# Optimization experiments

Hardware: AMD Instinct MI355X
Metric: run time of the kernel (lower is better)

Reference implementation:

```python
import jax, jax.numpy as jnp
import numpy as np


def setup_inputs() -> dict:
    key = jax.random.key(0)
    kK, kQ = jax.random.split(key)
    B, S, D = 8, 2048, 512
    K = jax.random.normal(kK, (B, S, D), dtype=jnp.float32)
    Q = jax.random.normal(kQ, (B, S, D), dtype=jnp.float32)
    return {"K": K, "Q": Q}


def reference(K, Q):
    # K: [B, S_k, D], Q: [B, S_q, D]
    S_q = Q.shape[1]
    S_k = K.shape[1]
    # Causal mask: -inf strictly above the diagonal (k=1), as in np.triu(..., k=1)
    mask = jnp.where(jnp.triu(jnp.ones((S_q, S_k), dtype=bool), k=1), -jnp.inf, 0.0).astype(jnp.float32)
    # NOTE: original scales by sqrt(window_size_keys) (seq len), and adds mask BEFORE scaling.
    logits = (jnp.einsum('bqd,bkd->bqk', Q, K) + mask) / jnp.sqrt(jnp.float32(S_k))
    return jax.nn.softmax(logits, axis=-1)
```

## Files before the change

### kernel.cpp

```cpp
#include <hip/hip_runtime.h>
#include <hip/hip_bf16.h>
#include <math.h>

#define B_SZ 8
#define SEQ 2048
#define DIM 512

typedef __attribute__((ext_vector_type(8))) short bf16x8;
typedef __attribute__((ext_vector_type(8))) unsigned short u16x8;
typedef __attribute__((ext_vector_type(4))) float f32x4;

#define GLOBAL_AS __attribute__((address_space(1)))
#define LDS_AS __attribute__((address_space(3)))

__device__ __forceinline__ unsigned short f2bf(float f) {
    unsigned int u = __builtin_bit_cast(unsigned int, f);
    u += 0x7fffu + ((u >> 16) & 1u);
    return (unsigned short)(u >> 16);
}

__device__ __forceinline__ void load_lds16(const void* g, void* l) {
    __builtin_amdgcn_global_load_lds((const GLOBAL_AS unsigned int*)g,
                                     (LDS_AS unsigned int*)l, 16, 0, 0);
}

__global__ __launch_bounds__(256)
void convert_kernel(const float* __restrict__ Q, const float* __restrict__ K,
                    unsigned short* __restrict__ Qb, unsigned short* __restrict__ Kb,
                    float* __restrict__ sums) {
    const int half = (int)(((size_t)B_SZ * SEQ * DIM) / 8 / 256);
    const int bid = blockIdx.x;
    const int gi = bid * 256 + threadIdx.x;
    if (gi < B_SZ * SEQ) sums[gi] = 0.f;

    const float* src;
    unsigned short* dst;
    int i;
    if (bid < half) { src = Q; dst = Qb; i = gi; }
    else            { src = K; dst = Kb; i = gi - half * 256; }

    const float4* s = (const float4*)src;
    float4 a = s[2 * i];
    float4 b = s[2 * i + 1];
    u16x8 o;
    o[0] = f2bf(a.x); o[1] = f2bf(a.y); o[2] = f2bf(a.z); o[3] = f2bf(a.w);
    o[4] = f2bf(b.x); o[5] = f2bf(b.y); o[6] = f2bf(b.z); o[7] = f2bf(b.w);
    ((u16x8*)dst)[i] = o;
}

#define BM 128
#define BK 32
__global__ __launch_bounds__(256)
void logits_exp_mfma(const unsigned short* __restrict__ Qb, const unsigned short* __restrict__ Kb,
                     float* __restrict__ out, float* __restrict__ sums) {
    const int b = blockIdx.x, tk = blockIdx.y, tq = blockIdx.z;
    float* outb = out + (size_t)b * SEQ * SEQ;
    const int t = threadIdx.x;

    if (tk > tq) {
        const int r0 = t >> 5;
        const int c4 = t & 31;
        const float4 z = {0.f, 0.f, 0.f, 0.f};
        float* base = outb + (size_t)(tq * BM) * SEQ + tk * BM;
#pragma unroll
        for (int it = 0; it < 16; ++it)
            *(float4*)(base + (size_t)(it * 8 + r0) * SEQ + c4 * 4) = z;
        return;
    }

    __shared__ __align__(16) unsigned short a_lds[BM * BK];
    __shared__ __align__(16) unsigned short b_lds[BM * BK];

    const int wave = t >> 6;
    const int lane = t & 63;
    const int l16 = lane & 15;
    const int quad = lane >> 4;
    const int wm = wave >> 1;
    const int wn = wave & 1;

    const unsigned short* Qrow = Qb + ((size_t)b * SEQ + (size_t)tq * BM) * DIM;
    const unsigned short* Krow = Kb + ((size_t)b * SEQ + (size_t)tk * BM) * DIM;

    const int sr = lane >> 2;
    const int kg = lane & 3;
    const int gsw = kg ^ ((sr >> 1) & 3);

    f32x4 acc[4][4];
#pragma unroll
    for (int i = 0; i < 4; i++)
#pragma unroll
        for (int j = 0; j < 4; j++) acc[i][j] = (f32x4){0.f, 0.f, 0.f, 0.f};

    for (int k0 = 0; k0 < DIM; k0 += BK) {
#pragma unroll
        for (int j = wave; j < 8; j += 4) {
            int row = j * 16 + sr;
            load_lds16(Qrow + (size_t)row * DIM + k0 + gsw * 8, &a_lds[(j * 16) * BK]);
            load_lds16(Krow + (size_t)row * DIM + k0 + gsw * 8, &b_lds[(j * 16) * BK]);
        }
        __syncthreads();

        bf16x8 af[4], bfr[4];
#pragma unroll
        for (int mi = 0; mi < 4; mi++) {
            const int row = wm * 64 + mi * 16 + l16;
            const int slot = quad ^ ((row >> 1) & 3);
            af[mi] = *(const bf16x8*)&a_lds[row * BK + slot * 8];
        }
#pragma unroll
        for (int ni = 0; ni < 4; ni++) {
            const int row = wn * 64 + ni * 16 + l16;
            const int slot = quad ^ ((row >> 1) & 3);
            bfr[ni] = *(const bf16x8*)&b_lds[row * BK + slot * 8];
        }
#pragma unroll
        for (int mi = 0; mi < 4; mi++)
#pragma unroll
            for (int ni = 0; ni < 4; ni++)
                acc[mi][ni] = __builtin_amdgcn_mfma_f32_16x16x32_bf16(af[mi], bfr[ni], acc[mi][ni], 0, 0, 0);
        __syncthreads();
    }

    const float scale = 0.02209708691207961f;
    const bool diag = (tk == tq);
    float* sums_b = sums + (size_t)b * SEQ;

#pragma unroll
    for (int mi = 0; mi < 4; mi++) {
#pragma unroll
        for (int r = 0; r < 4; r++) {
            const int row_l = wm * 64 + mi * 16 + quad * 4 + r;
            const int row = tq * BM + row_l;
            float rsum = 0.f;
#pragma unroll
            for (int ni = 0; ni < 4; ni++) {
                const int col = tk * BM + wn * 64 + ni * 16 + l16;
                float e;
                if (diag && col > row) e = 0.f;
                else e = __expf(acc[mi][ni][r] * scale);
                outb[(size_t)row * SEQ + col] = e;
                rsum += e;
            }
            rsum += __shfl_xor(rsum, 1);
            rsum += __shfl_xor(rsum, 2);
            rsum += __shfl_xor(rsum, 4);
            rsum += __shfl_xor(rsum, 8);
            if (l16 == 0) atomicAdd(&sums_b[row], rsum);
        }
    }
}

__global__ __launch_bounds__(256)
void scale_kernel(float* __restrict__ out, const float* __restrict__ sums) {
    const int q = blockIdx.x & (SEQ - 1);
    const int b = blockIdx.x >> 11;
    float* row = out + ((size_t)b * SEQ + q) * SEQ;
    const float inv = 1.0f / sums[blockIdx.x];
    const int n = q + 1;
    const int t = threadIdx.x;
#pragma unroll
    for (int j = 0; j < 2; ++j) {
        int k0 = (t + j * 256) * 4;
        if (k0 < n) {
            float4 x = *(const float4*)(row + k0);
            x.x *= inv; x.y *= inv; x.z *= inv; x.w *= inv;
            *(float4*)(row + k0) = x;
        }
    }
}

#define TS 64
#define DC 128
#define LSTRIDE (DC + 8)
__global__ __launch_bounds__(256)
void logits_fallback(const float* __restrict__ Q, const float* __restrict__ K,
                     float* __restrict__ out) {
    const int tk = blockIdx.x, tq = blockIdx.y, b = blockIdx.z;
    if (tk > tq) return;
    __shared__ __align__(16) unsigned short qs[TS * LSTRIDE];
    __shared__ __align__(16) unsigned short ks[TS * LSTRIDE];
    const int t = threadIdx.x;
    const int wave = t >> 6, lane = t & 63, l16 = lane & 15, quad = lane >> 4;
    const float* Qb = Q + ((size_t)b * SEQ + (size_t)tq * TS) * DIM;
    const float* Kb = K + ((size_t)b * SEQ + (size_t)tk * TS) * DIM;
    f32x4 acc[4];
#pragma unroll
    for (int i = 0; i < 4; i++) acc[i] = (f32x4){0.f, 0.f, 0.f, 0.f};
    for (int c = 0; c < DIM; c += DC) {
        __syncthreads();
#pragma unroll
        for (int i = 0; i < 8; i++) {
            int idx = t + i * 256;
            int row = idx >> 5, c4 = idx & 31;
            float4 qv = *(const float4*)(Qb + row * DIM + c + c4 * 4);
            float4 kv = *(const float4*)(Kb + row * DIM + c + c4 * 4);
            ushort4 qh = { f2bf(qv.x), f2bf(qv.y), f2bf(qv.z), f2bf(qv.w) };
            ushort4 kh = { f2bf(kv.x), f2bf(kv.y), f2bf(kv.z), f2bf(kv.w) };
            *(ushort4*)&qs[row * LSTRIDE + c4 * 4] = qh;
            *(ushort4*)&ks[row * LSTRIDE + c4 * 4] = kh;
        }
        __syncthreads();
#pragma unroll
        for (int d = 0; d < DC; d += 32) {
            bf16x8 afrag = *(const bf16x8*)&qs[(wave * 16 + l16) * LSTRIDE + d + quad * 8];
#pragma unroll
            for (int nt = 0; nt < 4; nt++) {
                bf16x8 bfrag = *(const bf16x8*)&ks[(nt * 16 + l16) * LSTRIDE + d + quad * 8];
                acc[nt] = __builtin_amdgcn_mfma_f32_16x16x32_bf16(afrag, bfrag, acc[nt], 0, 0, 0);
            }
        }
    }
    const float scale = 0.02209708691207961f;
    float* outb = out + (size_t)b * SEQ * SEQ;
#pragma unroll
    for (int nt = 0; nt < 4; nt++) {
        int col = tk * TS + nt * 16 + l16;
#pragma unroll
        for (int r = 0; r < 4; r++) {
            int row = tq * TS + wave * 16 + quad * 4 + r;
            outb[(size_t)row * SEQ + col] = acc[nt][r] * scale;
        }
    }
}

__global__ __launch_bounds__(256)
void softmax_kernel(float* __restrict__ out) {
    const int q = blockIdx.x & (SEQ - 1);
    const int b = blockIdx.x >> 11;
    float* row = out + ((size_t)b * SEQ + q) * SEQ;
    const int t = threadIdx.x;
    const int lane = t & 63;
    const int wave = t >> 6;
    const int n = q + 1;

    __shared__ float red[8];

    float4 v[2];
    float m = -INFINITY;
#pragma unroll
    for (int j = 0; j < 2; j++) {
        int k0 = (t + j * 256) * 4;
        if (k0 < n) {
            float4 x = *(const float4*)(row + k0);
            x.y = (k0 + 1 < n) ? x.y : -INFINITY;
            x.z = (k0 + 2 < n) ? x.z : -INFINITY;
            x.w = (k0 + 3 < n) ? x.w : -INFINITY;
            v[j] = x;
            m = fmaxf(m, fmaxf(fmaxf(x.x, x.y), fmaxf(x.z, x.w)));
        } else {
            v[j] = (float4){-INFINITY, -INFINITY, -INFINITY, -INFINITY};
        }
    }
#pragma unroll
    for (int off = 1; off < 64; off <<= 1) m = fmaxf(m, __shfl_xor(m, off));
    if (lane == 0) red[wave] = m;
    __syncthreads();
    m = fmaxf(fmaxf(red[0], red[1]), fmaxf(red[2], red[3]));

    float s = 0.f;
#pragma unroll
    for (int j = 0; j < 2; j++) {
        float4 e;
        e.x = __expf(v[j].x - m);
        e.y = __expf(v[j].y - m);
        e.z = __expf(v[j].z - m);
        e.w = __expf(v[j].w - m);
        v[j] = e;
        s += e.x + e.y + e.z + e.w;
    }
#pragma unroll
    for (int off = 1; off < 64; off <<= 1) s += __shfl_xor(s, off);
    if (lane == 0) red[4 + wave] = s;
    __syncthreads();
    s = red[4] + red[5] + red[6] + red[7];
    const float inv = 1.0f / s;

#pragma unroll
    for (int j = 0; j < 2; j++) {
        int k0 = (t + j * 256) * 4;
        float4 e = v[j];
        e.x *= inv; e.y *= inv; e.z *= inv; e.w *= inv;
        *(float4*)(row + k0) = e;
    }
}

extern "C" void kernel_launch(void* const* d_in, const int* in_sizes, int n_in,
                              void* d_out, int out_size, void* d_ws, size_t ws_size,
                              hipStream_t stream) {
    const float* Kp = (const float*)d_in[0];
    const float* Qp = (const float*)d_in[1];
    float* out = (float*)d_out;

    const size_t nElem = (size_t)B_SZ * SEQ * DIM;
    const size_t bfBytes = nElem * sizeof(unsigned short);
    const size_t sumsBytes = (size_t)B_SZ * SEQ * sizeof(float);

    if (ws_size >= 2 * bfBytes + sumsBytes) {
        unsigned short* Qbf = (unsigned short*)d_ws;
        unsigned short* Kbf = Qbf + nElem;
        float* sums = (float*)((char*)d_ws + 2 * bfBytes);
        const int half = (int)(nElem / 8 / 256);
        convert_kernel<<<dim3(2 * half), dim3(256), 0, stream>>>(Qp, Kp, Qbf, Kbf, sums);
        logits_exp_mfma<<<dim3(B_SZ, SEQ / BM, SEQ / BM), dim3(256), 0, stream>>>(Qbf, Kbf, out, sums);
        scale_kernel<<<dim3(B_SZ * SEQ), dim3(256), 0, stream>>>(out, sums);
    } else {
        logits_fallback<<<dim3(SEQ / TS, SEQ / TS, B_SZ), dim3(256), 0, stream>>>(Qp, Kp, out);
        softmax_kernel<<<dim3(B_SZ * SEQ), dim3(256), 0, stream>>>(out);
    }
}
```

Baseline: 227.4 us.

## Double-buffer LDS tiles to overlap global loads with MFMA compute

Turns the single LDS staging buffer for the Q and K tiles into a double buffer. The next K-slice is prefetched with global_load_lds while MFMAs run on the current slice, and a partial vmcnt wait (4 loads outstanding) replaces the full __syncthreads wait. This aims to hide global-memory latency in the GEMM main loop, at the cost of twice the LDS use, which may reduce occupancy. It also relies on hand-written waitcnt and barrier ordering being correct.

```diff
diff --git a/kernel.cpp b/kernel.cpp
--- a/kernel.cpp
+++ b/kernel.cpp
@@ -68,8 +68,8 @@
         return;
     }
 
-    __shared__ __align__(16) unsigned short a_lds[BM * BK];
-    __shared__ __align__(16) unsigned short b_lds[BM * BK];
+    __shared__ __align__(16) unsigned short a_lds[2][BM * BK];
+    __shared__ __align__(16) unsigned short b_lds[2][BM * BK];
 
     const int wave = t >> 6;
     const int lane = t & 63;
@@ -85,41 +85,59 @@
     const int kg = lane & 3;
     const int gsw = kg ^ ((sr >> 1) & 3);
 
+#define STAGE_TILE(bi, kt)                                                        \
+    {                                                                             \
+        _Pragma("unroll")                                                         \
+        for (int j = wave; j < 8; j += 4) {                                       \
+            int row = j * 16 + sr;                                                \
+            load_lds16(Qrow + (size_t)row * DIM + (kt) * BK + gsw * 8,            \
+                       &a_lds[bi][(j * 16) * BK]);                                \
+            load_lds16(Krow + (size_t)row * DIM + (kt) * BK + gsw * 8,            \
+                       &b_lds[bi][(j * 16) * BK]);                                \
+        }                                                                         \
+    }
+
     f32x4 acc[4][4];
 #pragma unroll
     for (int i = 0; i < 4; i++)
 #pragma unroll
         for (int j = 0; j < 4; j++) acc[i][j] = (f32x4){0.f, 0.f, 0.f, 0.f};
 
-    for (int k0 = 0; k0 < DIM; k0 += BK) {
-#pragma unroll
-        for (int j = wave; j < 8; j += 4) {
-            int row = j * 16 + sr;
-            load_lds16(Qrow + (size_t)row * DIM + k0 + gsw * 8, &a_lds[(j * 16) * BK]);
-            load_lds16(Krow + (size_t)row * DIM + k0 + gsw * 8, &b_lds[(j * 16) * BK]);
-        }
-        __syncthreads();
+    STAGE_TILE(0, 0);
+
+    for (int k = 0; k < 16; ++k) {
+        const int cur = k & 1;
+        if (k < 15) {
+            STAGE_TILE(cur ^ 1, k + 1);
+            asm volatile("s_waitcnt vmcnt(4)" ::: "memory");
+        } else {
+            asm volatile("s_waitcnt vmcnt(0)" ::: "memory");
+        }
+        __builtin_amdgcn_s_barrier();
 
         bf16x8 af[4], bfr[4];
 #pragma unroll
         for (int mi = 0; mi < 4; mi++) {
             const int row = wm * 64 + mi * 16 + l16;
             const int slot = quad ^ ((row >> 1) & 3);
-            af[mi] = *(const bf16x8*)&a_lds[row * BK + slot * 8];
+            af[mi] = *(const bf16x8*)&a_lds[cur][row * BK + slot * 8];
         }
 #pragma unroll
         for (int ni = 0; ni < 4; ni++) {
             const int row = wn * 64 + ni * 16 + l16;
             const int slot = quad ^ ((row >> 1) & 3);
-            bfr[ni] = *(const bf16x8*)&b_lds[row * BK + slot * 8];
+            bfr[ni] = *(const bf16x8*)&b_lds[cur][row * BK + slot * 8];
         }
 #pragma unroll
         for (int mi = 0; mi < 4; mi++)
 #pragma unroll
             for (int ni = 0; ni < 4; ni++)
                 acc[mi][ni] = __builtin_amdgcn_mfma_f32_16x16x32_bf16(af[mi], bfr[ni], acc[mi][ni], 0, 0, 0);
-        __syncthreads();
-    }
+
+        __builtin_amdgcn_s_barrier();
+        __builtin_amdgcn_sched_barrier(0);
+    }
+#undef STAGE_TILE
 
     const float scale = 0.02209708691207961f;
     const bool diag = (tk == tq);
```

Result: no change. 227.6 us (+0.1%).
